# Optimization experiments

Hardware: AMD Instinct MI355X
Metric: run time of the kernel (lower is better)

## Reference

```python
import jax, jax.numpy as jnp
import numpy as np

B, S, T = 16, 256, 2048
V, D, H, L, FF, NM = 3000, 512, 8, 6, 2048, 80
DH = D // H


def _make_pe(max_len=5000, d=D):
    pos = np.arange(max_len, dtype=np.float32)[:, None]
    div = np.exp(np.arange(0, d, 2, dtype=np.float32) * (-np.log(10000.0) / d))
    pe = np.zeros((max_len, d), dtype=np.float32)
    pe[:, 0::2] = np.sin(pos * div)
    pe[:, 1::2] = np.cos(pos * div)
    return jnp.asarray(pe[None])  # [1, max_len, D]


def setup_inputs() -> dict:
    key = jax.random.key(0)
    ks = jax.random.split(key, 24)
    f = jnp.float32
    n = lambda k, sh, s=0.02: jax.random.normal(k, sh, f) * s
    return {
        'text_ids': jax.random.randint(ks[0], (B, S), 0, V),
        'text_lengths': jax.random.randint(ks[1], (B,), S // 2, S + 1),
        'mel_targets': jax.random.normal(ks[2], (B, NM, T), f),
        'emb': n(ks[3], (V, D), 0.05),
        'pe': _make_pe(),
        'Wqkv': n(ks[4], (L, D, 3 * D)), 'bqkv': jnp.zeros((L, 3 * D), f),
        'Wo': n(ks[5], (L, D, D)), 'bo': jnp.zeros((L, D), f),
        'ln1_s': jnp.ones((L, D), f), 'ln1_b': jnp.zeros((L, D), f),
        'ln2_s': jnp.ones((L, D), f), 'ln2_b': jnp.zeros((L, D), f),
        'W1': n(ks[6], (L, D, FF)), 'b1': jnp.zeros((L, FF), f),
        'W2': n(ks[7], (L, FF, D)), 'b2': jnp.zeros((L, D), f),
        'mel_W1': n(ks[8], (D, FF)), 'mel_b1': jnp.zeros((FF,), f),
        'mel_W2': n(ks[9], (FF, NM)), 'mel_b2': jnp.zeros((NM,), f),
        'dur_W1': n(ks[10], (D, 256)), 'dur_b1': jnp.zeros((256,), f),
        'dur_W2': n(ks[11], (256, 1)), 'dur_b2': jnp.zeros((1,), f),
    }


def _layer_norm(x, s, b, eps=1e-5):
    m = jnp.mean(x, -1, keepdims=True)
    v = jnp.mean(jnp.square(x - m), -1, keepdims=True)
    return (x - m) * jax.lax.rsqrt(v + eps) * s + b


def _length_regulate(enc, durations, target_len):
    # enc [B,S,D], durations [B,S] -> [B,target_len,D]
    dur = jnp.maximum(jnp.round(durations).astype(jnp.int32), 1)
    cum = jnp.cumsum(dur, axis=1)                              # [B,S] inclusive
    pos = jnp.arange(target_len)                               # [T]
    idx = jnp.sum(pos[None, None, :] >= cum[:, :, None], axis=1)  # [B,T]
    idx = jnp.minimum(idx, enc.shape[1] - 1)
    valid = pos[None, :] < cum[:, -1:]                         # [B,T]
    out = jnp.take_along_axis(enc, idx[..., None], axis=1)
    return out * valid[..., None].astype(enc.dtype)


def reference(text_ids, text_lengths, mel_targets, emb, pe, Wqkv, bqkv, Wo, bo,
              ln1_s, ln1_b, ln2_s, ln2_b, W1, b1, W2, b2,
              mel_W1, mel_b1, mel_W2, mel_b2, dur_W1, dur_b1, dur_W2, dur_b2):
    x = emb[text_ids] + pe[:, :S]                              # [B,S,D]
    pad = jnp.arange(S)[None, :] >= text_lengths[:, None]      # True = padded key
    bias = jnp.where(pad, -1e9, 0.0)[:, None, None, :]         # [B,1,1,S]
    scale = 1.0 / jnp.sqrt(jnp.float32(DH))
    for l in range(L):
        qkv = x @ Wqkv[l] + bqkv[l]
        q, k, v = jnp.split(qkv, 3, axis=-1)
        q = q.reshape(B, S, H, DH).transpose(0, 2, 1, 3)
        k = k.reshape(B, S, H, DH).transpose(0, 2, 1, 3)
        v = v.reshape(B, S, H, DH).transpose(0, 2, 1, 3)
        scores = jnp.einsum('bhqd,bhkd->bhqk', q, k) * scale + bias
        attn = jax.nn.softmax(scores, axis=-1)
        o = jnp.einsum('bhqk,bhkd->bhqd', attn, v)
        o = o.transpose(0, 2, 1, 3).reshape(B, S, D) @ Wo[l] + bo[l]
        x = _layer_norm(x + o, ln1_s[l], ln1_b[l])              # post-LN (torch default)
        ff = jax.nn.relu(x @ W1[l] + b1[l]) @ W2[l] + b2[l]
        x = _layer_norm(x + ff, ln2_s[l], ln2_b[l])
    enc = x
    dur_h = jax.nn.relu(enc @ dur_W1 + dur_b1)
    durations = jax.nn.softplus((dur_h @ dur_W2 + dur_b2).squeeze(-1))  # [B,S]
    target_len = mel_targets.shape[2]
    expanded = _length_regulate(enc, durations, target_len)    # [B,T,D]
    mel = jax.nn.relu(expanded @ mel_W1 + mel_b1) @ mel_W2 + mel_b2
    mel = mel.transpose(0, 2, 1)                               # [B,NM,T]
    return mel, durations, enc
```

## Files before the change

kernel.cpp:

```cpp
#include <hip/hip_runtime.h>
#include <math.h>

#define B_ 16
#define S_ 256
#define T_ 2048
#define D_ 512
#define H_ 8
#define L_ 6
#define FF_ 2048
#define NM_ 80
#define M_ 4096

typedef float floatx4 __attribute__((ext_vector_type(4)));
typedef __bf16 bf16x8 __attribute__((ext_vector_type(8)));
typedef unsigned short u16x8 __attribute__((ext_vector_type(8)));

__device__ __forceinline__ float bf2f(unsigned u) {
    return __uint_as_float((u & 0xffffu) << 16);
}
__device__ __forceinline__ unsigned short f2bf(float f) {
    unsigned u = __float_as_uint(f);
    unsigned r = u + 0x7fffu + ((u >> 16) & 1u);
    return (unsigned short)(r >> 16);
}
__device__ __forceinline__ void gload_lds16(const void* g, void* l) {
    __builtin_amdgcn_global_load_lds(
        (const __attribute__((address_space(1))) void*)g,
        (__attribute__((address_space(3))) void*)l, 16, 0, 0);
}

__device__ __forceinline__ void tr_body(
    const float* __restrict__ src, unsigned short* __restrict__ dst,
    int K, int N, int bx, int by, int bz, float (*tile)[33], int Ns )
{
    const int k0 = by * 32, n0 = bx * 32;
    src += (size_t)bz * K * Ns;
    dst += (size_t)bz * K * N;
    const int tid = threadIdx.x;
    const int tx = tid & 31, ty = tid >> 5;
#pragma unroll
    for (int i = 0; i < 32; i += 8) {
        int n = n0 + tx;
        tile[ty + i][tx] = (n < Ns) ? src[(size_t)(k0 + ty + i) * Ns + n] : 0.f;
    }
    __syncthreads();
    const int tx2 = tid & 15, ty2 = tid >> 4;
#pragma unroll
    for (int i = 0; i < 32; i += 16) {
        unsigned lo = f2bf(tile[2 * tx2][ty2 + i]);
        unsigned hi = f2bf(tile[2 * tx2 + 1][ty2 + i]);
        *(unsigned*)(dst + (size_t)(n0 + ty2 + i) * K + k0 + 2 * tx2) = lo | (hi << 16);
    }
}

__global__ __launch_bounds__(256) void prep_weights(
    const float* __restrict__ Wqkv, const float* __restrict__ Wo,
    const float* __restrict__ W1, const float* __restrict__ W2,
    const float* __restrict__ melW1, const float* __restrict__ melW2,
    const float* __restrict__ durW1, const float* __restrict__ melb1,
    const float* __restrict__ melb2, const float* __restrict__ durb1,
    unsigned short* __restrict__ Wqkv_t, unsigned short* __restrict__ Wo_t,
    unsigned short* __restrict__ W1_t, unsigned short* __restrict__ W2_t,
    unsigned short* __restrict__ wcomb, unsigned short* __restrict__ melW2_t,
    float* __restrict__ cbias, float* __restrict__ c0)
{
    __shared__ float tile[32][33];
    int bid = blockIdx.x;
    if (bid < 4608) {
        int z = bid / 768, r = bid % 768;
        tr_body(Wqkv, Wqkv_t, 512, 1536, r % 48, r / 48, z, tile, 1536);
        return;
    }
    bid -= 4608;
    if (bid < 1536) {
        int z = bid / 256, r = bid % 256;
        tr_body(Wo, Wo_t, 512, 512, r % 16, r / 16, z, tile, 512);
        return;
    }
    bid -= 1536;
    if (bid < 6144) {
        int z = bid / 1024, r = bid % 1024;
        tr_body(W1, W1_t, 512, 2048, r % 64, r / 64, z, tile, 2048);
        return;
    }
    bid -= 6144;
    if (bid < 6144) {
        int z = bid / 1024, r = bid % 1024;
        tr_body(W2, W2_t, 2048, 512, r % 16, r / 16, z, tile, 512);
        return;
    }
    bid -= 6144;
    if (bid < 1024) {
        tr_body(melW1, wcomb, 512, 2304, bid % 64, bid / 64, 0, tile, 2048);
        return;
    }
    bid -= 1024;
    if (bid < 256) {
        tr_body(melW2, melW2_t, 2048, 128, bid % 4, bid / 4, 0, tile, 80);
        return;
    }
    bid -= 256;
    if (bid < 128) {
        tr_body(durW1, wcomb + (size_t)2048 * 512, 512, 256, bid % 8, bid / 8, 0, tile, 256);
        return;
    }
    bid -= 128;
    if (bid < 9) {
        int idx = bid * 256 + threadIdx.x;
        cbias[idx] = (idx < 2048) ? melb1[idx] : durb1[idx - 2048];
        return;
    }
    bid -= 9;
    {
        float* red = (float*)tile;
        const int c = bid;
        const int tid = threadIdx.x;
        float p = 0.f;
        for (int f = tid; f < 2048; f += 256)
            p += fmaxf(melb1[f], 0.f) * melW2[(size_t)f * 80 + c];
#pragma unroll
        for (int off = 32; off >= 1; off >>= 1) p += __shfl_xor(p, off, 64);
        if ((tid & 63) == 0) red[tid >> 6] = p;
        __syncthreads();
        if (tid == 0) c0[c] = red[0] + red[1] + red[2] + red[3] + melb2[c];
    }
}

__global__ __launch_bounds__(128) void embed_bf16(
    const int* __restrict__ ids, const float* __restrict__ emb,
    const float* __restrict__ pe, unsigned short* __restrict__ x)
{
    const int r = blockIdx.x;
    const int c = threadIdx.x * 4;
    const int id = ids[r];
    const int s = r & (S_ - 1);
    float4 e = *(const float4*)(emb + (size_t)id * D_ + c);
    float4 p = *(const float4*)(pe + (size_t)s * D_ + c);
    ushort4 o;
    o.x = f2bf(e.x + p.x); o.y = f2bf(e.y + p.y);
    o.z = f2bf(e.z + p.z); o.w = f2bf(e.w + p.w);
    *(ushort4*)(x + (size_t)r * D_ + c) = o;
}

template<int BM, int BN>
__global__ __launch_bounds__(256) void gemm2(
    const unsigned short* __restrict__ A, const unsigned short* __restrict__ Bt,
    const float* __restrict__ bias, unsigned short* __restrict__ Cb,
    float* __restrict__ Cpart, unsigned short* __restrict__ vtp,
    int N, int klen, int act, int lda)
{
    constexpr int NSUB_A = BM / 8;
    constexpr int NSUB_B = BN / 8;
    constexpr int NSUB = NSUB_A + NSUB_B;
    constexpr int NL = NSUB / 4;
    constexpr int BUFSZ = NSUB * 1024;
    constexpr int AOFF = NSUB_A * 1024;
    constexpr int WM = BM / 32, WN = BN / 32;
    __shared__ __attribute__((aligned(16))) char smem[2 * BUFSZ];

    const int tid = threadIdx.x;
    const int wave = tid >> 6, lane = tid & 63;
    const int lm = lane & 15, quad = lane >> 4;
    const int wm = wave >> 1, wn = wave & 1;
    const int m0 = blockIdx.y * BM;
    const int n0 = blockIdx.x * BN;
    const int Kfull = klen * gridDim.z;
    const int kb = blockIdx.z * klen;

    floatx4 acc[WM][WN];
#pragma unroll
    for (int i = 0; i < WM; i++)
#pragma unroll
        for (int j = 0; j < WN; j++) acc[i][j] = (floatx4){0.f, 0.f, 0.f, 0.f};

    const unsigned short* ga[NL];
    int loff[NL];
#pragma unroll
    for (int j = 0; j < NL; j++) {
        int sid = wave * NL + j;
        if (sid < NSUB_A) {
            int mi = sid >> 1, ki = sid & 1;
            ga[j] = A + (size_t)(m0 + mi * 16 + lm) * lda + kb + ki * 32 + quad * 8;
            loff[j] = sid * 1024;
        } else {
            int t = sid - NSUB_A;
            int ni = t >> 1, ki = t & 1;
            ga[j] = Bt + (size_t)(n0 + ni * 16 + lm) * Kfull + kb + ki * 32 + quad * 8;
            loff[j] = AOFF + t * 1024;
        }
    }

#pragma unroll
    for (int j = 0; j < NL; j++) gload_lds16(ga[j], smem + loff[j]);

    for (int kt = 0; kt < klen; kt += 64) {
        char* sc = smem + ((kt >> 6) & 1) * BUFSZ;
        if (kt + 64 < klen) {
            char* sn = smem + (((kt >> 6) + 1) & 1) * BUFSZ;
#pragma unroll
            for (int j = 0; j < NL; j++) gload_lds16(ga[j] + kt + 64, sn + loff[j]);
            __builtin_amdgcn_s_waitcnt(0x0F70 | NL);
        } else {
            __builtin_amdgcn_s_waitcnt(0x0F70);
        }
        asm volatile("" ::: "memory");
        __builtin_amdgcn_s_barrier();
        asm volatile("" ::: "memory");

#pragma unroll
        for (int ki = 0; ki < 2; ki++) {
            bf16x8 af[WM], bfr[WN];
#pragma unroll
            for (int i = 0; i < WM; i++)
                af[i] = *(const bf16x8*)(sc + ((((wm * WM + i) * 2 + ki) << 10) + (lane << 4)));
#pragma unroll
            for (int j = 0; j < WN; j++)
                bfr[j] = *(const bf16x8*)(sc + AOFF + ((((wn * WN + j) * 2 + ki) << 10) + (lane << 4)));
#pragma unroll
            for (int i = 0; i < WM; i++)
#pragma unroll
                for (int j = 0; j < WN; j++)
                    acc[i][j] = __builtin_amdgcn_mfma_f32_16x16x32_bf16(
                        af[i], bfr[j], acc[i][j], 0, 0, 0);
        }
        asm volatile("" ::: "memory");
        __builtin_amdgcn_s_barrier();
        asm volatile("" ::: "memory");
    }

    if constexpr (BM == 128 && BN == 128) {
        if (vtp != nullptr && n0 >= 1024) {
            unsigned short* sT = (unsigned short*)smem;
#pragma unroll
            for (int mi = 0; mi < WM; mi++) {
                const int rl = wm * 64 + mi * 16 + quad * 4;
#pragma unroll
                for (int nj = 0; nj < WN; nj++) {
                    const int cl = wn * 64 + nj * 16 + lm;
                    const float bv = bias[n0 + cl];
                    ushort4 t4;
                    t4.x = f2bf(acc[mi][nj][0] + bv);
                    t4.y = f2bf(acc[mi][nj][1] + bv);
                    t4.z = f2bf(acc[mi][nj][2] + bv);
                    t4.w = f2bf(acc[mi][nj][3] + bv);
                    *(ushort4*)(sT + cl * 136 + rl) = t4;
                }
            }
            __syncthreads();
            const int b = m0 >> 8;
            const int s0 = m0 & 255;
            const int h0 = (n0 - 1024) >> 6;
#pragma unroll
            for (int i = 0; i < 8; i++) {
                int idx = i * 256 + tid;
                int d = idx >> 4, c = idx & 15;
                uint4 v = *(const uint4*)(sT + d * 136 + c * 8);
                int bh = b * 8 + h0 + (d >> 6);
                *(uint4*)(vtp + ((size_t)bh * 64 + (d & 63)) * 256 + s0 + c * 8) = v;
            }
            return;
        }
    }

    if (gridDim.z == 1) {
#pragma unroll
        for (int mi = 0; mi < WM; mi++) {
            const int rb = m0 + wm * (WM * 16) + mi * 16 + quad * 4;
#pragma unroll
            for (int nj = 0; nj < WN; nj++) {
                const int col = n0 + wn * (WN * 16) + nj * 16 + lm;
                const float bv = bias[col];
#pragma unroll
                for (int r = 0; r < 4; r++) {
                    float o = acc[mi][nj][r] + bv;
                    if (act) o = fmaxf(o, 0.f);
                    Cb[(size_t)(rb + r) * N + col] = f2bf(o);
                }
            }
        }
    } else {
        float* Cp = Cpart + (size_t)blockIdx.z * gridDim.y * BM * N;
#pragma unroll
        for (int mi = 0; mi < WM; mi++) {
            const int rb = m0 + wm * (WM * 16) + mi * 16 + quad * 4;
#pragma unroll
            for (int nj = 0; nj < WN; nj++) {
                const int col = n0 + wn * (WN * 16) + nj * 16 + lm;
#pragma unroll
                for (int r = 0; r < 4; r++)
                    Cp[(size_t)(rb + r) * N + col] = acc[mi][nj][r];
            }
        }
    }
}

__global__ __launch_bounds__(64) void attn_fused(
    const unsigned short* __restrict__ qkv, const unsigned short* __restrict__ vt,
    const int* __restrict__ lens, unsigned short* __restrict__ o)
{
    __shared__ __attribute__((aligned(16))) unsigned short sP[16 * 280];
    const int lane = threadIdx.x;
    const int lm = lane & 15, quad = lane >> 4;
    const int qt = blockIdx.x;
    const int bh = blockIdx.y;
    const int b = bh >> 3, h = bh & 7;
    const int len = lens[b];
    const unsigned short* Qb = qkv + ((size_t)b * 256 + qt * 16) * 1536 + h * 64;
    const unsigned short* Kb = qkv + (size_t)b * 256 * 1536 + 512 + h * 64;
    const unsigned short* Vt = vt + (size_t)bh * 64 * 256;

    bf16x8 aq0 = *(const bf16x8*)(Qb + (size_t)lm * 1536 + quad * 8);
    bf16x8 aq1 = *(const bf16x8*)(Qb + (size_t)lm * 1536 + 32 + quad * 8);

    floatx4 accS[16];
#pragma unroll
    for (int nf = 0; nf < 16; nf++) accS[nf] = (floatx4){0.f, 0.f, 0.f, 0.f};

#pragma unroll
    for (int nf = 0; nf < 16; nf++) {
        const unsigned short* kr = Kb + (size_t)(nf * 16 + lm) * 1536 + quad * 8;
        bf16x8 bk0 = *(const bf16x8*)(kr);
        bf16x8 bk1 = *(const bf16x8*)(kr + 32);
        accS[nf] = __builtin_amdgcn_mfma_f32_16x16x32_bf16(aq0, bk0, accS[nf], 0, 0, 0);
        accS[nf] = __builtin_amdgcn_mfma_f32_16x16x32_bf16(aq1, bk1, accS[nf], 0, 0, 0);
    }

    float lrow[4];
    const float scale = 0.125f;
#pragma unroll
    for (int r = 0; r < 4; r++) {
        float sum = 0.f;
#pragma unroll
        for (int nf = 0; nf < 16; nf++) {
            float s = accS[nf][r] * scale + ((nf * 16 + lm >= len) ? -1e9f : 0.f);
            float e = __expf(s);
            accS[nf][r] = e;
            sum += e;
        }
#pragma unroll
        for (int off = 1; off < 16; off <<= 1) sum += __shfl_xor(sum, off, 64);
        lrow[r] = sum;
    }

#pragma unroll
    for (int nf = 0; nf < 16; nf++) {
        const int col = nf * 16 + lm;
#pragma unroll
        for (int r = 0; r < 4; r++)
            sP[(quad * 4 + r) * 280 + col] = f2bf(accS[nf][r]);
    }

    floatx4 accO[4];
#pragma unroll
    for (int nj = 0; nj < 4; nj++) accO[nj] = (floatx4){0.f, 0.f, 0.f, 0.f};

#pragma unroll
    for (int ks = 0; ks < 8; ks++) {
        bf16x8 ap = *(const bf16x8*)(sP + lm * 280 + ks * 32 + quad * 8);
#pragma unroll
        for (int nj = 0; nj < 4; nj++) {
            bf16x8 bv = *(const bf16x8*)(Vt + (size_t)(nj * 16 + lm) * 256
                                         + ks * 32 + quad * 8);
            accO[nj] = __builtin_amdgcn_mfma_f32_16x16x32_bf16(ap, bv, accO[nj], 0, 0, 0);
        }
    }

    float inv[4];
#pragma unroll
    for (int r = 0; r < 4; r++) inv[r] = 1.f / lrow[r];
    const int grow = b * 256 + qt * 16 + quad * 4;
#pragma unroll
    for (int nj = 0; nj < 4; nj++) {
        const int gcol = h * 64 + nj * 16 + lm;
#pragma unroll
        for (int r = 0; r < 4; r++)
            o[(size_t)(grow + r) * 512 + gcol] = f2bf(accO[nj][r] * inv[r]);
    }
}

__global__ __launch_bounds__(512) void add_ln_bf16(
    unsigned short* __restrict__ x, const unsigned short* __restrict__ y,
    const float* __restrict__ s, const float* __restrict__ bb)
{
    const int wave = threadIdx.x >> 6, lane = threadIdx.x & 63;
    const int row = blockIdx.x * 8 + wave;
    const int c = lane * 8;
    u16x8 xv = *(const u16x8*)(x + (size_t)row * D_ + c);
    u16x8 yv = *(const u16x8*)(y + (size_t)row * D_ + c);
    float h[8];
    float sum = 0.f;
#pragma unroll
    for (int j = 0; j < 8; j++) {
        h[j] = bf2f(xv[j]) + bf2f(yv[j]);
        sum += h[j];
    }
#pragma unroll
    for (int off = 32; off >= 1; off >>= 1) sum += __shfl_xor(sum, off, 64);
    float mean = sum * (1.f / 512.f);

    float d[8], sq = 0.f;
#pragma unroll
    for (int j = 0; j < 8; j++) {
        d[j] = h[j] - mean;
        sq += d[j] * d[j];
    }
#pragma unroll
    for (int off = 32; off >= 1; off >>= 1) sq += __shfl_xor(sq, off, 64);
    float rs = rsqrtf(sq * (1.f / 512.f) + 1e-5f);

    float4 sv0 = *(const float4*)(s + c), sv1 = *(const float4*)(s + c + 4);
    float4 bv0 = *(const float4*)(bb + c), bv1 = *(const float4*)(bb + c + 4);
    u16x8 ov;
    ov[0] = f2bf(d[0] * rs * sv0.x + bv0.x);
    ov[1] = f2bf(d[1] * rs * sv0.y + bv0.y);
    ov[2] = f2bf(d[2] * rs * sv0.z + bv0.z);
    ov[3] = f2bf(d[3] * rs * sv0.w + bv0.w);
    ov[4] = f2bf(d[4] * rs * sv1.x + bv1.x);
    ov[5] = f2bf(d[5] * rs * sv1.y + bv1.y);
    ov[6] = f2bf(d[6] * rs * sv1.z + bv1.z);
    ov[7] = f2bf(d[7] * rs * sv1.w + bv1.w);
    *(u16x8*)(x + (size_t)row * D_ + c) = ov;
}

__global__ __launch_bounds__(512) void add_ln_part(
    unsigned short* __restrict__ x, const float* __restrict__ p0,
    const float* __restrict__ p1, const float* __restrict__ bias,
    const float* __restrict__ s, const float* __restrict__ bb,
    float* __restrict__ enc_opt)
{
    const int wave = threadIdx.x >> 6, lane = threadIdx.x & 63;
    const int row = blockIdx.x * 8 + wave;
    const int c = lane * 8;
    u16x8 xv = *(const u16x8*)(x + (size_t)row * D_ + c);
    float4 a0 = *(const float4*)(p0 + (size_t)row * D_ + c);
    float4 a1 = *(const float4*)(p0 + (size_t)row * D_ + c + 4);
    float4 q0 = *(const float4*)(p1 + (size_t)row * D_ + c);
    float4 q1 = *(const float4*)(p1 + (size_t)row * D_ + c + 4);
    float4 bi0 = *(const float4*)(bias + c);
    float4 bi1 = *(const float4*)(bias + c + 4);
    float h[8];
    h[0] = bf2f(xv[0]) + a0.x + q0.x + bi0.x;
    h[1] = bf2f(xv[1]) + a0.y + q0.y + bi0.y;
    h[2] = bf2f(xv[2]) + a0.z + q0.z + bi0.z;
    h[3] = bf2f(xv[3]) + a0.w + q0.w + bi0.w;
    h[4] = bf2f(xv[4]) + a1.x + q1.x + bi1.x;
    h[5] = bf2f(xv[5]) + a1.y + q1.y + bi1.y;
    h[6] = bf2f(xv[6]) + a1.z + q1.z + bi1.z;
    h[7] = bf2f(xv[7]) + a1.w + q1.w + bi1.w;

    float sum = 0.f;
#pragma unroll
    for (int j = 0; j < 8; j++) sum += h[j];
#pragma unroll
    for (int off = 32; off >= 1; off >>= 1) sum += __shfl_xor(sum, off, 64);
    float mean = sum * (1.f / 512.f);

    float d[8], sq = 0.f;
#pragma unroll
    for (int j = 0; j < 8; j++) {
        d[j] = h[j] - mean;
        sq += d[j] * d[j];
    }
#pragma unroll
    for (int off = 32; off >= 1; off >>= 1) sq += __shfl_xor(sq, off, 64);
    float rs = rsqrtf(sq * (1.f / 512.f) + 1e-5f);

    float4 sv0 = *(const float4*)(s + c), sv1 = *(const float4*)(s + c + 4);
    float4 bv0 = *(const float4*)(bb + c), bv1 = *(const float4*)(bb + c + 4);
    float o[8];
    o[0] = d[0] * rs * sv0.x + bv0.x;
    o[1] = d[1] * rs * sv0.y + bv0.y;
    o[2] = d[2] * rs * sv0.z + bv0.z;
    o[3] = d[3] * rs * sv0.w + bv0.w;
    o[4] = d[4] * rs * sv1.x + bv1.x;
    o[5] = d[5] * rs * sv1.y + bv1.y;
    o[6] = d[6] * rs * sv1.z + bv1.z;
    o[7] = d[7] * rs * sv1.w + bv1.w;
    u16x8 ov;
#pragma unroll
    for (int j = 0; j < 8; j++) ov[j] = f2bf(o[j]);
    *(u16x8*)(x + (size_t)row * D_ + c) = ov;
    if (enc_opt) {
        float4 e0, e1;
        e0.x = o[0]; e0.y = o[1]; e0.z = o[2]; e0.w = o[3];
        e1.x = o[4]; e1.y = o[5]; e1.z = o[6]; e1.w = o[7];
        *(float4*)(enc_opt + (size_t)row * D_ + c) = e0;
        *(float4*)(enc_opt + (size_t)row * D_ + c + 4) = e1;
    }
}

__global__ __launch_bounds__(256) void dur_rows(
    const unsigned short* __restrict__ hcomb, const float* __restrict__ w2,
    const float* __restrict__ b2, float* __restrict__ durout,
    int* __restrict__ dint)
{
    const int tid = threadIdx.x;
    const int w = tid >> 6, lane = tid & 63;
    const int r = blockIdx.x * 4 + w;
    ushort4 hv = *(const ushort4*)(hcomb + (size_t)r * 2304 + 2048 + lane * 4);
    float4 wv = *(const float4*)(w2 + lane * 4);
    float p = bf2f(hv.x) * wv.x + bf2f(hv.y) * wv.y
            + bf2f(hv.z) * wv.z + bf2f(hv.w) * wv.w;
#pragma unroll
    for (int off = 32; off >= 1; off >>= 1) p += __shfl_xor(p, off, 64);
    if (lane == 0) {
        float v = p + b2[0];
        float dur = (v > 20.f) ? v : log1pf(expf(v));
        durout[r] = dur;
        int d = (int)rintf(dur);
        if (d < 1) d = 1;
        dint[r] = d;
    }
}

__global__ __launch_bounds__(256) void dur_scan(
    const int* __restrict__ dint, int* __restrict__ cum)
{
    __shared__ int sd[256];
    const int tid = threadIdx.x;
    const int b = blockIdx.x;
    sd[tid] = dint[b * 256 + tid];
    __syncthreads();
    for (int off = 1; off < 256; off <<= 1) {
        int v = sd[tid];
        int add = (tid >= off) ? sd[tid - off] : 0;
        __syncthreads();
        sd[tid] = v + add;
        __syncthreads();
    }
    cum[b * 256 + tid] = sd[tid];
}

__global__ __launch_bounds__(256) void mel_combine(
    const float* __restrict__ mp, const float* __restrict__ b2,
    float* __restrict__ melc)
{
    const int idx = blockIdx.x * 256 + threadIdx.x;
    const int r = idx / 80, c = idx - r * 80;
    const size_t plane = (size_t)M_ * 128;
    const size_t base = (size_t)r * 128 + c;
    melc[idx] = mp[base] + mp[plane + base] + mp[2 * plane + base]
              + mp[3 * plane + base] + b2[c];
}

__global__ __launch_bounds__(256) void mel_gather2(
    const float* __restrict__ melc, const float* __restrict__ c0,
    const int* __restrict__ cum, float* __restrict__ mel_out)
{
    __shared__ float rows[256 * 40];
    __shared__ int sc[256];
    __shared__ float s0[40];
    const int tid = threadIdx.x;
    const int b = blockIdx.z;
    const int cc0 = blockIdx.y * 40;
    sc[tid] = cum[b * 256 + tid];
    if (tid < 40) s0[tid] = c0[cc0 + tid];
    for (int idx = tid; idx < 256 * 40; idx += 256) {
        int r = idx / 40, c = idx - r * 40;
        rows[idx] = melc[((size_t)b * 256 + r) * 80 + cc0 + c];
    }
    __syncthreads();
    const int total = sc[255];
    const int t = blockIdx.x * 256 + tid;
    int lo = 0, hi = 256;
    while (lo < hi) {
        int mid = (lo + hi) >> 1;
        if (sc[mid] <= t) lo = mid + 1; else hi = mid;
    }
    int row = lo < 255 ? lo : 255;
    const bool valid = t < total;
    const float* src = valid ? &rows[row * 40] : s0;
    for (int cc = 0; cc < 40; cc++)
        mel_out[((size_t)b * 80 + cc0 + cc) * T_ + t] = src[cc];
}

extern "C" void kernel_launch(void* const* d_in, const int* in_sizes, int n_in,
                              void* d_out, int out_size, void* d_ws, size_t ws_size,
                              hipStream_t stream)
{
    const int*   text_ids     = (const int*)d_in[0];
    const int*   text_lengths = (const int*)d_in[1];
    const float* emb   = (const float*)d_in[3];
    const float* pe    = (const float*)d_in[4];
    const float* Wqkv  = (const float*)d_in[5];
    const float* bqkv  = (const float*)d_in[6];
    const float* Wo    = (const float*)d_in[7];
    const float* bo    = (const float*)d_in[8];
    const float* ln1_s = (const float*)d_in[9];
    const float* ln1_b = (const float*)d_in[10];
    const float* ln2_s = (const float*)d_in[11];
    const float* ln2_b = (const float*)d_in[12];
    const float* W1    = (const float*)d_in[13];
    const float* b1    = (const float*)d_in[14];
    const float* W2    = (const float*)d_in[15];
    const float* b2    = (const float*)d_in[16];
    const float* mel_W1 = (const float*)d_in[17];
    const float* mel_b1 = (const float*)d_in[18];
    const float* mel_W2 = (const float*)d_in[19];
    const float* mel_b2 = (const float*)d_in[20];
    const float* dur_W1 = (const float*)d_in[21];
    const float* dur_b1 = (const float*)d_in[22];
    const float* dur_W2 = (const float*)d_in[23];
    const float* dur_b2 = (const float*)d_in[24];

    float* out = (float*)d_out;
    float* mel_out = out;
    float* dur_out = out + (size_t)B_ * NM_ * T_;
    float* enc_out = dur_out + (size_t)B_ * S_;

    typedef unsigned short u16;
    char* w = (char*)d_ws;
    u16* Wqkv_t  = (u16*)w;                   w += (size_t)L_ * 1536 * 512 * 2;
    u16* Wo_t    = (u16*)w;                   w += (size_t)L_ * 512 * 512 * 2;
    u16* W1_t    = (u16*)w;                   w += (size_t)L_ * 2048 * 512 * 2;
    u16* W2_t    = (u16*)w;                   w += (size_t)L_ * 512 * 2048 * 2;
    u16* wcomb   = (u16*)w;                   w += (size_t)2304 * 512 * 2;
    u16* melW2_t = (u16*)w;                   w += (size_t)128 * 2048 * 2;
    u16* x_bf    = (u16*)w;                   w += (size_t)M_ * 512 * 2;
    u16* qkv_bf  = (u16*)w;                   w += (size_t)M_ * 1536 * 2;
    u16* ao_bf   = (u16*)w;                   w += (size_t)M_ * 512 * 2;
    u16* y_bf    = (u16*)w;                   w += (size_t)M_ * 512 * 2;
    char* big    = w;                         w += (size_t)18874368;
    float* c0    = (float*)w;                 w += 512;
    int*   cum   = (int*)w;                   w += (size_t)M_ * 4;
    int*   dint  = (int*)w;                   w += (size_t)M_ * 4;
    float* cbias = (float*)w;                 w += (size_t)2304 * 4;
    float* melc  = (float*)w;                 w += (size_t)M_ * 80 * 4;

    u16* ffh     = (u16*)big;
    u16* hcomb   = (u16*)big;
    u16* vt      = (u16*)(big + 12582912);

    float* part2 = (float*)qkv_bf;
    float* mpart = (float*)(qkv_bf + (size_t)M_ * 512);

    prep_weights<<<19929, 256, 0, stream>>>(
        Wqkv, Wo, W1, W2, mel_W1, mel_W2, dur_W1, mel_b1, mel_b2, dur_b1,
        Wqkv_t, Wo_t, W1_t, W2_t, wcomb, melW2_t, cbias, c0);

    embed_bf16<<<M_, 128, 0, stream>>>(text_ids, emb, pe, x_bf);

    for (int l = 0; l < L_; l++) {
        gemm2<128, 128><<<dim3(12, 32), 256, 0, stream>>>(
            x_bf, Wqkv_t + (size_t)l * 1536 * 512, bqkv + (size_t)l * 1536,
            qkv_bf, nullptr, vt, 1536, 512, 0, 512);
        attn_fused<<<dim3(16, 128), 64, 0, stream>>>(qkv_bf, vt, text_lengths, ao_bf);
        gemm2<128, 64><<<dim3(8, 32), 256, 0, stream>>>(
            ao_bf, Wo_t + (size_t)l * 512 * 512, bo + (size_t)l * 512,
            y_bf, nullptr, nullptr, 512, 512, 0, 512);
        add_ln_bf16<<<M_ / 8, 512, 0, stream>>>(
            x_bf, y_bf, ln1_s + (size_t)l * D_, ln1_b + (size_t)l * D_);
        gemm2<128, 128><<<dim3(16, 32), 256, 0, stream>>>(
            x_bf, W1_t + (size_t)l * 2048 * 512, b1 + (size_t)l * 2048,
            ffh, nullptr, nullptr, 2048, 512, 1, 512);
        gemm2<128, 64><<<dim3(8, 32, 2), 256, 0, stream>>>(
            ffh, W2_t + (size_t)l * 512 * 2048, nullptr,
            nullptr, part2, nullptr, 512, 1024, 0, 2048);
        add_ln_part<<<M_ / 8, 512, 0, stream>>>(
            x_bf, part2, part2 + (size_t)M_ * 512, b2 + (size_t)l * 512,
            ln2_s + (size_t)l * D_, ln2_b + (size_t)l * D_,
            (l == L_ - 1) ? enc_out : nullptr);
    }

    gemm2<128, 128><<<dim3(18, 32), 256, 0, stream>>>(
        x_bf, wcomb, cbias, hcomb, nullptr, nullptr, 2304, 512, 1, 512);

    dur_rows<<<M_ / 4, 256, 0, stream>>>(hcomb, dur_W2, dur_b2, dur_out, dint);
    dur_scan<<<B_, 256, 0, stream>>>(dint, cum);

    gemm2<128, 64><<<dim3(2, 32, 4), 256, 0, stream>>>(
        hcomb, melW2_t, nullptr, nullptr, mpart, nullptr, 128, 512, 0, 2304);
    mel_combine<<<1280, 256, 0, stream>>>(mpart, mel_b2, melc);
    mel_gather2<<<dim3(T_ / 256, 2, B_), 256, 0, stream>>>(melc, c0, cum, mel_out);
}
```

Baseline: 881.9 us.

## Stage K in LDS and process 128 query rows per attention block

Attention blocks now cover 128 query rows with 4 waves (32 rows each) instead of 16 rows with one wave. The whole K tile for the head is staged once into shared memory with direct global-to-LDS loads and reused by all waves, and the P·V product runs in two halves to keep the LDS footprint small. This is meant to cut redundant global K reads and reuse each V fragment across two row tiles. In exchange there are fewer blocks (256 instead of 2048), higher register pressure from doubled accumulators, and extra barriers.

```diff
diff --git a/kernel.cpp b/kernel.cpp
--- a/kernel.cpp
+++ b/kernel.cpp
@@ -294,87 +294,126 @@
     }
 }
 
-__global__ __launch_bounds__(64) void attn_fused(
+__global__ __launch_bounds__(256) void attn_fused(
     const unsigned short* __restrict__ qkv, const unsigned short* __restrict__ vt,
     const int* __restrict__ lens, unsigned short* __restrict__ o)
 {
-    __shared__ __attribute__((aligned(16))) unsigned short sP[16 * 280];
-    const int lane = threadIdx.x;
+    __shared__ __attribute__((aligned(16))) char smem[34816];
+    const int tid = threadIdx.x;
+    const int wave = tid >> 6, lane = tid & 63;
     const int lm = lane & 15, quad = lane >> 4;
     const int qt = blockIdx.x;
     const int bh = blockIdx.y;
     const int b = bh >> 3, h = bh & 7;
     const int len = lens[b];
-    const unsigned short* Qb = qkv + ((size_t)b * 256 + qt * 16) * 1536 + h * 64;
+    const unsigned short* Qb = qkv + ((size_t)b * 256 + qt * 128) * 1536 + h * 64;
     const unsigned short* Kb = qkv + (size_t)b * 256 * 1536 + 512 + h * 64;
     const unsigned short* Vt = vt + (size_t)bh * 64 * 256;
 
-    bf16x8 aq0 = *(const bf16x8*)(Qb + (size_t)lm * 1536 + quad * 8);
-    bf16x8 aq1 = *(const bf16x8*)(Qb + (size_t)lm * 1536 + 32 + quad * 8);
-
-    floatx4 accS[16];
-#pragma unroll
-    for (int nf = 0; nf < 16; nf++) accS[nf] = (floatx4){0.f, 0.f, 0.f, 0.f};
+#pragma unroll
+    for (int j = 0; j < 8; j++) {
+        int sid = wave * 8 + j;
+        int nf = sid >> 1, kf = sid & 1;
+        gload_lds16(Kb + (size_t)(nf * 16 + lm) * 1536 + kf * 32 + quad * 8,
+                    smem + sid * 1024);
+    }
+    bf16x8 aq[2][2];
+#pragma unroll
+    for (int mi = 0; mi < 2; mi++)
+#pragma unroll
+        for (int kf = 0; kf < 2; kf++)
+            aq[mi][kf] = *(const bf16x8*)(Qb + (size_t)(wave * 32 + mi * 16 + lm) * 1536
+                                          + kf * 32 + quad * 8);
+    __syncthreads();
+
+    floatx4 accS[2][16];
+#pragma unroll
+    for (int mi = 0; mi < 2; mi++)
+#pragma unroll
+        for (int nf = 0; nf < 16; nf++) accS[mi][nf] = (floatx4){0.f, 0.f, 0.f, 0.f};
 
 #pragma unroll
     for (int nf = 0; nf < 16; nf++) {
-        const unsigned short* kr = Kb + (size_t)(nf * 16 + lm) * 1536 + quad * 8;
-        bf16x8 bk0 = *(const bf16x8*)(kr);
-        bf16x8 bk1 = *(const bf16x8*)(kr + 32);
-        accS[nf] = __builtin_amdgcn_mfma_f32_16x16x32_bf16(aq0, bk0, accS[nf], 0, 0, 0);
-        accS[nf] = __builtin_amdgcn_mfma_f32_16x16x32_bf16(aq1, bk1, accS[nf], 0, 0, 0);
-    }
-
-    float lrow[4];
+        bf16x8 bk0 = *(const bf16x8*)(smem + (nf * 2 + 0) * 1024 + lane * 16);
+        bf16x8 bk1 = *(const bf16x8*)(smem + (nf * 2 + 1) * 1024 + lane * 16);
+        accS[0][nf] = __builtin_amdgcn_mfma_f32_16x16x32_bf16(aq[0][0], bk0, accS[0][nf], 0, 0, 0);
+        accS[0][nf] = __builtin_amdgcn_mfma_f32_16x16x32_bf16(aq[0][1], bk1, accS[0][nf], 0, 0, 0);
+        accS[1][nf] = __builtin_amdgcn_mfma_f32_16x16x32_bf16(aq[1][0], bk0, accS[1][nf], 0, 0, 0);
+        accS[1][nf] = __builtin_amdgcn_mfma_f32_16x16x32_bf16(aq[1][1], bk1, accS[1][nf], 0, 0, 0);
+    }
+
+    float lrow[2][4];
     const float scale = 0.125f;
 #pragma unroll
-    for (int r = 0; r < 4; r++) {
-        float sum = 0.f;
-#pragma unroll
-        for (int nf = 0; nf < 16; nf++) {
-            float s = accS[nf][r] * scale + ((nf * 16 + lm >= len) ? -1e9f : 0.f);
-            float e = __expf(s);
-            accS[nf][r] = e;
-            sum += e;
-        }
-#pragma unroll
-        for (int off = 1; off < 16; off <<= 1) sum += __shfl_xor(sum, off, 64);
-        lrow[r] = sum;
-    }
-
-#pragma unroll
-    for (int nf = 0; nf < 16; nf++) {
-        const int col = nf * 16 + lm;
-#pragma unroll
-        for (int r = 0; r < 4; r++)
-            sP[(quad * 4 + r) * 280 + col] = f2bf(accS[nf][r]);
-    }
-
-    floatx4 accO[4];
-#pragma unroll
-    for (int nj = 0; nj < 4; nj++) accO[nj] = (floatx4){0.f, 0.f, 0.f, 0.f};
-
-#pragma unroll
-    for (int ks = 0; ks < 8; ks++) {
-        bf16x8 ap = *(const bf16x8*)(sP + lm * 280 + ks * 32 + quad * 8);
+    for (int mi = 0; mi < 2; mi++)
+#pragma unroll
+        for (int r = 0; r < 4; r++) {
+            float sum = 0.f;
+#pragma unroll
+            for (int nf = 0; nf < 16; nf++) {
+                float s = accS[mi][nf][r] * scale + ((nf * 16 + lm >= len) ? -1e9f : 0.f);
+                float e = __expf(s);
+                accS[mi][nf][r] = e;
+                sum += e;
+            }
+#pragma unroll
+            for (int off = 1; off < 16; off <<= 1) sum += __shfl_xor(sum, off, 64);
+            lrow[mi][r] = sum;
+        }
+
+    floatx4 accO[2][4];
+#pragma unroll
+    for (int mi = 0; mi < 2; mi++)
+#pragma unroll
+        for (int nj = 0; nj < 4; nj++) accO[mi][nj] = (floatx4){0.f, 0.f, 0.f, 0.f};
+
+    __syncthreads();
+    unsigned short* sP = (unsigned short*)smem;
+    const int rbase = wave * 32;
+#pragma unroll
+    for (int half = 0; half < 2; half++) {
+#pragma unroll
+        for (int mi = 0; mi < 2; mi++)
+#pragma unroll
+            for (int nf2 = 0; nf2 < 8; nf2++) {
+                int nf = half * 8 + nf2;
+                int row = rbase + mi * 16 + quad * 4;
+                int col = nf2 * 16 + lm;
+#pragma unroll
+                for (int r = 0; r < 4; r++)
+                    sP[(row + r) * 136 + col] = f2bf(accS[mi][nf][r]);
+            }
+#pragma unroll
+        for (int ks2 = 0; ks2 < 4; ks2++) {
+            bf16x8 ap[2];
+#pragma unroll
+            for (int mi = 0; mi < 2; mi++)
+                ap[mi] = *(const bf16x8*)(sP + (rbase + mi * 16 + lm) * 136
+                                          + ks2 * 32 + quad * 8);
+            int ks = half * 4 + ks2;
+#pragma unroll
+            for (int nj = 0; nj < 4; nj++) {
+                bf16x8 bv = *(const bf16x8*)(Vt + (size_t)(nj * 16 + lm) * 256
+                                             + ks * 32 + quad * 8);
+                accO[0][nj] = __builtin_amdgcn_mfma_f32_16x16x32_bf16(ap[0], bv, accO[0][nj], 0, 0, 0);
+                accO[1][nj] = __builtin_amdgcn_mfma_f32_16x16x32_bf16(ap[1], bv, accO[1][nj], 0, 0, 0);
+            }
+        }
+    }
+
+#pragma unroll
+    for (int mi = 0; mi < 2; mi++) {
+        float inv[4];
+#pragma unroll
+        for (int r = 0; r < 4; r++) inv[r] = 1.f / lrow[mi][r];
+        const int grow = b * 256 + qt * 128 + rbase + mi * 16 + quad * 4;
 #pragma unroll
         for (int nj = 0; nj < 4; nj++) {
-            bf16x8 bv = *(const bf16x8*)(Vt + (size_t)(nj * 16 + lm) * 256
-                                         + ks * 32 + quad * 8);
-            accO[nj] = __builtin_amdgcn_mfma_f32_16x16x32_bf16(ap, bv, accO[nj], 0, 0, 0);
-        }
-    }
-
-    float inv[4];
-#pragma unroll
-    for (int r = 0; r < 4; r++) inv[r] = 1.f / lrow[r];
-    const int grow = b * 256 + qt * 16 + quad * 4;
-#pragma unroll
-    for (int nj = 0; nj < 4; nj++) {
-        const int gcol = h * 64 + nj * 16 + lm;
-#pragma unroll
-        for (int r = 0; r < 4; r++)
-            o[(size_t)(grow + r) * 512 + gcol] = f2bf(accO[nj][r] * inv[r]);
+            const int gcol = h * 64 + nj * 16 + lm;
+#pragma unroll
+            for (int r = 0; r < 4; r++)
+                o[(size_t)(grow + r) * 512 + gcol] = f2bf(accO[mi][nj][r] * inv[r]);
+        }
     }
 }
 
@@ -644,7 +683,7 @@
         gemm2<128, 128><<<dim3(12, 32), 256, 0, stream>>>(
             x_bf, Wqkv_t + (size_t)l * 1536 * 512, bqkv + (size_t)l * 1536,
             qkv_bf, nullptr, vt, 1536, 512, 0, 512);
-        attn_fused<<<dim3(16, 128), 64, 0, stream>>>(qkv_bf, vt, text_lengths, ao_bf);
+        attn_fused<<<dim3(2, 128), 256, 0, stream>>>(qkv_bf, vt, text_lengths, ao_bf);
         gemm2<128, 64><<<dim3(8, 32), 256, 0, stream>>>(
             ao_bf, Wo_t + (size_t)l * 512 * 512, bo + (size_t)l * 512,
             y_bf, nullptr, nullptr, 512, 512, 0, 512);
```

New measurement: 836.9 us. 5.1% less time.

## Share K tile across four waves in attention and merge tail kernels

Applied to the files above, without the earlier changes.

The attention kernel now runs four waves per block, each covering 16 query rows of a 64-row tile. K for the head is staged once into LDS via async global-to-LDS loads, so it is no longer reloaded from global memory by every 16-row wave. The duration row reduction and the mel partial combine are merged into one launch. The duration prefix scan moves into mel_gather2, which drops two tiny launches but repeats the scan in every gather block. LDS per attention block grows to 34 KB, which may limit occupancy.

```diff
diff --git a/kernel.cpp b/kernel.cpp
--- a/kernel.cpp
+++ b/kernel.cpp
@@ -294,23 +294,35 @@
     }
 }
 
-__global__ __launch_bounds__(64) void attn_fused(
+__global__ __launch_bounds__(256) void attn_fused(
     const unsigned short* __restrict__ qkv, const unsigned short* __restrict__ vt,
     const int* __restrict__ lens, unsigned short* __restrict__ o)
 {
-    __shared__ __attribute__((aligned(16))) unsigned short sP[16 * 280];
-    const int lane = threadIdx.x;
+    __shared__ __attribute__((aligned(16))) char smem[34816];
+    const int tid = threadIdx.x;
+    const int wave = tid >> 6, lane = tid & 63;
     const int lm = lane & 15, quad = lane >> 4;
     const int qt = blockIdx.x;
     const int bh = blockIdx.y;
     const int b = bh >> 3, h = bh & 7;
     const int len = lens[b];
-    const unsigned short* Qb = qkv + ((size_t)b * 256 + qt * 16) * 1536 + h * 64;
+    const unsigned short* Qb = qkv + ((size_t)b * 256 + qt * 64) * 1536 + h * 64;
     const unsigned short* Kb = qkv + (size_t)b * 256 * 1536 + 512 + h * 64;
     const unsigned short* Vt = vt + (size_t)bh * 64 * 256;
 
-    bf16x8 aq0 = *(const bf16x8*)(Qb + (size_t)lm * 1536 + quad * 8);
-    bf16x8 aq1 = *(const bf16x8*)(Qb + (size_t)lm * 1536 + 32 + quad * 8);
+#pragma unroll
+    for (int j = 0; j < 8; j++) {
+        int sid = wave * 8 + j;
+        int nf = sid >> 1, kf = sid & 1;
+        gload_lds16(Kb + (size_t)(nf * 16 + lm) * 1536 + kf * 32 + quad * 8,
+                    smem + sid * 1024);
+    }
+    bf16x8 aq[2];
+#pragma unroll
+    for (int kf = 0; kf < 2; kf++)
+        aq[kf] = *(const bf16x8*)(Qb + (size_t)(wave * 16 + lm) * 1536
+                                  + kf * 32 + quad * 8);
+    __syncthreads();
 
     floatx4 accS[16];
 #pragma unroll
@@ -318,11 +330,10 @@
 
 #pragma unroll
     for (int nf = 0; nf < 16; nf++) {
-        const unsigned short* kr = Kb + (size_t)(nf * 16 + lm) * 1536 + quad * 8;
-        bf16x8 bk0 = *(const bf16x8*)(kr);
-        bf16x8 bk1 = *(const bf16x8*)(kr + 32);
-        accS[nf] = __builtin_amdgcn_mfma_f32_16x16x32_bf16(aq0, bk0, accS[nf], 0, 0, 0);
-        accS[nf] = __builtin_amdgcn_mfma_f32_16x16x32_bf16(aq1, bk1, accS[nf], 0, 0, 0);
+        bf16x8 bk0 = *(const bf16x8*)(smem + (nf * 2 + 0) * 1024 + lane * 16);
+        bf16x8 bk1 = *(const bf16x8*)(smem + (nf * 2 + 1) * 1024 + lane * 16);
+        accS[nf] = __builtin_amdgcn_mfma_f32_16x16x32_bf16(aq[0], bk0, accS[nf], 0, 0, 0);
+        accS[nf] = __builtin_amdgcn_mfma_f32_16x16x32_bf16(aq[1], bk1, accS[nf], 0, 0, 0);
     }
 
     float lrow[4];
@@ -342,21 +353,24 @@
         lrow[r] = sum;
     }
 
+    floatx4 accO[4];
+#pragma unroll
+    for (int nj = 0; nj < 4; nj++) accO[nj] = (floatx4){0.f, 0.f, 0.f, 0.f};
+
+    __syncthreads();
+    unsigned short* sP = (unsigned short*)smem;
+    const int rbase = wave * 16;
 #pragma unroll
     for (int nf = 0; nf < 16; nf++) {
+        const int row = rbase + quad * 4;
         const int col = nf * 16 + lm;
 #pragma unroll
         for (int r = 0; r < 4; r++)
-            sP[(quad * 4 + r) * 280 + col] = f2bf(accS[nf][r]);
-    }
-
-    floatx4 accO[4];
-#pragma unroll
-    for (int nj = 0; nj < 4; nj++) accO[nj] = (floatx4){0.f, 0.f, 0.f, 0.f};
-
+            sP[(row + r) * 264 + col] = f2bf(accS[nf][r]);
+    }
 #pragma unroll
     for (int ks = 0; ks < 8; ks++) {
-        bf16x8 ap = *(const bf16x8*)(sP + lm * 280 + ks * 32 + quad * 8);
+        bf16x8 ap = *(const bf16x8*)(sP + (rbase + lm) * 264 + ks * 32 + quad * 8);
 #pragma unroll
         for (int nj = 0; nj < 4; nj++) {
             bf16x8 bv = *(const bf16x8*)(Vt + (size_t)(nj * 16 + lm) * 256
@@ -368,7 +382,7 @@
     float inv[4];
 #pragma unroll
     for (int r = 0; r < 4; r++) inv[r] = 1.f / lrow[r];
-    const int grow = b * 256 + qt * 16 + quad * 4;
+    const int grow = b * 256 + qt * 64 + rbase + quad * 4;
 #pragma unroll
     for (int nj = 0; nj < 4; nj++) {
         const int gcol = h * 64 + nj * 16 + lm;
@@ -489,63 +503,46 @@
     }
 }
 
-__global__ __launch_bounds__(256) void dur_rows(
+__global__ __launch_bounds__(256) void head_aux(
     const unsigned short* __restrict__ hcomb, const float* __restrict__ w2,
-    const float* __restrict__ b2, float* __restrict__ durout,
-    int* __restrict__ dint)
+    const float* __restrict__ b2d, float* __restrict__ durout,
+    int* __restrict__ dint,
+    const float* __restrict__ mp, const float* __restrict__ b2m,
+    float* __restrict__ melc)
 {
     const int tid = threadIdx.x;
-    const int w = tid >> 6, lane = tid & 63;
-    const int r = blockIdx.x * 4 + w;
-    ushort4 hv = *(const ushort4*)(hcomb + (size_t)r * 2304 + 2048 + lane * 4);
-    float4 wv = *(const float4*)(w2 + lane * 4);
-    float p = bf2f(hv.x) * wv.x + bf2f(hv.y) * wv.y
-            + bf2f(hv.z) * wv.z + bf2f(hv.w) * wv.w;
-#pragma unroll
-    for (int off = 32; off >= 1; off >>= 1) p += __shfl_xor(p, off, 64);
-    if (lane == 0) {
-        float v = p + b2[0];
-        float dur = (v > 20.f) ? v : log1pf(expf(v));
-        durout[r] = dur;
-        int d = (int)rintf(dur);
-        if (d < 1) d = 1;
-        dint[r] = d;
-    }
-}
-
-__global__ __launch_bounds__(256) void dur_scan(
-    const int* __restrict__ dint, int* __restrict__ cum)
-{
-    __shared__ int sd[256];
-    const int tid = threadIdx.x;
-    const int b = blockIdx.x;
-    sd[tid] = dint[b * 256 + tid];
-    __syncthreads();
-    for (int off = 1; off < 256; off <<= 1) {
-        int v = sd[tid];
-        int add = (tid >= off) ? sd[tid - off] : 0;
-        __syncthreads();
-        sd[tid] = v + add;
-        __syncthreads();
-    }
-    cum[b * 256 + tid] = sd[tid];
-}
-
-__global__ __launch_bounds__(256) void mel_combine(
-    const float* __restrict__ mp, const float* __restrict__ b2,
-    float* __restrict__ melc)
-{
-    const int idx = blockIdx.x * 256 + threadIdx.x;
+    int bid = blockIdx.x;
+    if (bid < 1024) {
+        const int w = tid >> 6, lane = tid & 63;
+        const int r = bid * 4 + w;
+        ushort4 hv = *(const ushort4*)(hcomb + (size_t)r * 2304 + 2048 + lane * 4);
+        float4 wv = *(const float4*)(w2 + lane * 4);
+        float p = bf2f(hv.x) * wv.x + bf2f(hv.y) * wv.y
+                + bf2f(hv.z) * wv.z + bf2f(hv.w) * wv.w;
+#pragma unroll
+        for (int off = 32; off >= 1; off >>= 1) p += __shfl_xor(p, off, 64);
+        if (lane == 0) {
+            float v = p + b2d[0];
+            float dur = (v > 20.f) ? v : log1pf(expf(v));
+            durout[r] = dur;
+            int d = (int)rintf(dur);
+            if (d < 1) d = 1;
+            dint[r] = d;
+        }
+        return;
+    }
+    bid -= 1024;
+    const int idx = bid * 256 + tid;
     const int r = idx / 80, c = idx - r * 80;
     const size_t plane = (size_t)M_ * 128;
     const size_t base = (size_t)r * 128 + c;
     melc[idx] = mp[base] + mp[plane + base] + mp[2 * plane + base]
-              + mp[3 * plane + base] + b2[c];
+              + mp[3 * plane + base] + b2m[c];
 }
 
 __global__ __launch_bounds__(256) void mel_gather2(
     const float* __restrict__ melc, const float* __restrict__ c0,
-    const int* __restrict__ cum, float* __restrict__ mel_out)
+    const int* __restrict__ dint, float* __restrict__ mel_out)
 {
     __shared__ float rows[256 * 40];
     __shared__ int sc[256];
@@ -553,13 +550,20 @@
     const int tid = threadIdx.x;
     const int b = blockIdx.z;
     const int cc0 = blockIdx.y * 40;
-    sc[tid] = cum[b * 256 + tid];
+    sc[tid] = dint[b * 256 + tid];
     if (tid < 40) s0[tid] = c0[cc0 + tid];
     for (int idx = tid; idx < 256 * 40; idx += 256) {
         int r = idx / 40, c = idx - r * 40;
         rows[idx] = melc[((size_t)b * 256 + r) * 80 + cc0 + c];
     }
     __syncthreads();
+    for (int off = 1; off < 256; off <<= 1) {
+        int v = sc[tid];
+        int add = (tid >= off) ? sc[tid - off] : 0;
+        __syncthreads();
+        sc[tid] = v + add;
+        __syncthreads();
+    }
     const int total = sc[255];
     const int t = blockIdx.x * 256 + tid;
     int lo = 0, hi = 256;
@@ -622,7 +626,6 @@
     u16* y_bf    = (u16*)w;                   w += (size_t)M_ * 512 * 2;
     char* big    = w;                         w += (size_t)18874368;
     float* c0    = (float*)w;                 w += 512;
-    int*   cum   = (int*)w;                   w += (size_t)M_ * 4;
     int*   dint  = (int*)w;                   w += (size_t)M_ * 4;
     float* cbias = (float*)w;                 w += (size_t)2304 * 4;
     float* melc  = (float*)w;                 w += (size_t)M_ * 80 * 4;
@@ -644,7 +647,7 @@
         gemm2<128, 128><<<dim3(12, 32), 256, 0, stream>>>(
             x_bf, Wqkv_t + (size_t)l * 1536 * 512, bqkv + (size_t)l * 1536,
             qkv_bf, nullptr, vt, 1536, 512, 0, 512);
-        attn_fused<<<dim3(16, 128), 64, 0, stream>>>(qkv_bf, vt, text_lengths, ao_bf);
+        attn_fused<<<dim3(4, 128), 256, 0, stream>>>(qkv_bf, vt, text_lengths, ao_bf);
         gemm2<128, 64><<<dim3(8, 32), 256, 0, stream>>>(
             ao_bf, Wo_t + (size_t)l * 512 * 512, bo + (size_t)l * 512,
             y_bf, nullptr, nullptr, 512, 512, 0, 512);
@@ -665,11 +668,9 @@
     gemm2<128, 128><<<dim3(18, 32), 256, 0, stream>>>(
         x_bf, wcomb, cbias, hcomb, nullptr, nullptr, 2304, 512, 1, 512);
 
-    dur_rows<<<M_ / 4, 256, 0, stream>>>(hcomb, dur_W2, dur_b2, dur_out, dint);
-    dur_scan<<<B_, 256, 0, stream>>>(dint, cum);
-
     gemm2<128, 64><<<dim3(2, 32, 4), 256, 0, stream>>>(
         hcomb, melW2_t, nullptr, nullptr, mpart, nullptr, 128, 512, 0, 2304);
-    mel_combine<<<1280, 256, 0, stream>>>(mpart, mel_b2, melc);
-    mel_gather2<<<dim3(T_ / 256, 2, B_), 256, 0, stream>>>(melc, c0, cum, mel_out);
-}
+    head_aux<<<2304, 256, 0, stream>>>(
+        hcomb, dur_W2, dur_b2, dur_out, dint, mpart, mel_b2, melc);
+    mel_gather2<<<dim3(T_ / 256, 2, B_), 256, 0, stream>>>(melc, c0, dint, mel_out);
+}
```

Result: faster. 858.4 us (-2.7%).
